# Optimization experiments

Hardware: AMD Instinct MI355X
Metric: run time of the kernel (lower is better)

The kernel has to match this reference:

```python
import jax, jax.numpy as jnp
import numpy as np

NUM_HEADS = 16
HEAD_DIM = 64
HIDDEN = NUM_HEADS * HEAD_DIM  # 1024
B, T = 32, 512


def setup_inputs() -> dict:
    key = jax.random.key(0)
    ks = jax.random.split(key, 10)
    s = 1.0 / np.sqrt(HIDDEN)
    inp = {
        "x": jax.random.normal(ks[0], (B, HIDDEN, T), dtype=jnp.float32),
        "mask": jax.random.randint(ks[1], (B, T), 0, 2, dtype=jnp.int32),
        "Wq": jax.random.uniform(ks[2], (HIDDEN, HIDDEN), jnp.float32, -s, s),
        "bq": jax.random.uniform(ks[3], (HIDDEN,), jnp.float32, -s, s),
        "Wk": jax.random.uniform(ks[4], (HIDDEN, HIDDEN), jnp.float32, -s, s),
        "bk": jax.random.uniform(ks[5], (HIDDEN,), jnp.float32, -s, s),
        "Wv": jax.random.uniform(ks[6], (HIDDEN, HIDDEN), jnp.float32, -s, s),
        "bv": jax.random.uniform(ks[7], (HIDDEN,), jnp.float32, -s, s),
        "Wo": jax.random.uniform(ks[8], (HIDDEN, HIDDEN), jnp.float32, -s, s),
        "bo": jax.random.uniform(ks[9], (HIDDEN,), jnp.float32, -s, s),
    }
    return inp


def reference(x, mask, Wq, bq, Wk, bk, Wv, bv, Wo, bo):
    # x: [B, hidden, T] -> tokens along last axis
    b, h, t = x.shape
    xt = jnp.swapaxes(x, 1, 2)  # [B, T, hidden]

    def heads(w, bias):
        y = xt @ w.T + bias                       # [B, T, hidden]
        return y.reshape(b, t, NUM_HEADS, HEAD_DIM).transpose(0, 2, 1, 3)  # [B, nh, T, hd]

    q = heads(Wq, bq)
    k = heads(Wk, bk)
    v = heads(Wv, bv)

    scores = jnp.einsum("bhqd,bhkd->bhqk", q, k) / jnp.sqrt(jnp.float32(HEAD_DIM))
    # masked_fill(mask==0, -inf) then clamp to [-50, 50]: masked entries become -50
    scores = jnp.where(mask[:, None, None, :] == 0, -jnp.inf, scores)
    scores = jnp.clip(scores, -50.0, 50.0)
    attn = jax.nn.softmax(scores, axis=-1)        # [B, nh, T, T]
    out = jnp.einsum("bhqk,bhkd->bhqd", attn, v)  # [B, nh, T, hd]
    out = out.transpose(0, 2, 1, 3).reshape(b, t, h)
    out = out @ Wo.T + bo                         # [B, T, hidden]
    return out.max(axis=1)                        # [B, hidden]
```

## Files before the change

kernel.cpp:

```cpp
#include <hip/hip_runtime.h>


typedef _Float16 half8 __attribute__((ext_vector_type(8)));
typedef _Float16 half4 __attribute__((ext_vector_type(4)));
typedef float floatx4 __attribute__((ext_vector_type(4)));
typedef unsigned uintx2 __attribute__((ext_vector_type(2)));

#define HID 1024
#define TT 512
#define NB 32
#define QSCALE 0.1803368801111244f
#define SB2 72.13475204444817f

__device__ __forceinline__ void gload16(const void* g, void* l) {
    __builtin_amdgcn_global_load_lds(
        (const __attribute__((address_space(1))) unsigned int*)g,
        (__attribute__((address_space(3))) unsigned int*)l, 16, 0, 0);
}

__device__ __forceinline__ unsigned fkey(float f) {
    unsigned u = __float_as_uint(f);
    return (u & 0x80000000u) ? ~u : (u | 0x80000000u);
}
__device__ __forceinline__ float funkey(unsigned k) {
    unsigned u = (k & 0x80000000u) ? (k ^ 0x80000000u) : ~k;
    return __uint_as_float(u);
}

__global__ __launch_bounds__(256) void prep_kernel(
    const float* __restrict__ Wq, const float* __restrict__ Wk,
    const float* __restrict__ Wv, const float* __restrict__ Wo,
    _Float16* __restrict__ Wcat,
    const float* __restrict__ x, _Float16* __restrict__ xT,
    unsigned* __restrict__ omax,
    const float* __restrict__ bq, float* __restrict__ bqs)
{
    __shared__ float tile[64][65];
    const int bid = blockIdx.x;
    if (bid < 4096) {
        int i4 = bid * 256 + threadIdx.x;
        int sec = i4 >> 18;
        int off4 = i4 & ((1 << 18) - 1);
        const float* src = (sec == 0) ? Wq : (sec == 1) ? Wk
                          : (sec == 2) ? Wv : Wo;
        float4 v = ((const float4*)src)[off4];
        if (sec == 0) {
            v.x *= QSCALE; v.y *= QSCALE; v.z *= QSCALE; v.w *= QSCALE;
        }
        half4 h = {(_Float16)v.x, (_Float16)v.y, (_Float16)v.z, (_Float16)v.w};
        *(half4*)(Wcat + (size_t)i4 * 4) = h;
    } else if (bid < 8192) {
        int idx = bid - 4096;
        int b = idx >> 7, h0 = ((idx >> 3) & 15) * 64, t0 = (idx & 7) * 64;
        int tx = threadIdx.x & 15, ty = threadIdx.x >> 4;
        const float* xb = x + ((size_t)b * HID + h0) * TT + t0;
        for (int p = 0; p < 4; p++) {
            int r = ty + 16 * p;
            float4 v = *(const float4*)(xb + (size_t)r * TT + tx * 4);
            tile[r][tx * 4 + 0] = v.x;
            tile[r][tx * 4 + 1] = v.y;
            tile[r][tx * 4 + 2] = v.z;
            tile[r][tx * 4 + 3] = v.w;
        }
        __syncthreads();
        int hc = (threadIdx.x & 7) * 8, tb = threadIdx.x >> 3;
        for (int rd = 0; rd < 2; rd++) {
            int tt = tb + 32 * rd;
            half8 pk;
            for (int k = 0; k < 8; k++)
                pk[k] = (_Float16)tile[hc + k][tt];
            *(half8*)(xT + ((size_t)b * TT + t0 + tt) * HID + h0 + hc) = pk;
        }
    } else if (bid < 8320) {
        omax[(bid - 8192) * 256 + threadIdx.x] = 0u;
    } else {
        int i = (bid - 8320) * 256 + threadIdx.x;
        bqs[i] = bq[i] * QSCALE;
    }
}


#define PH_PRE do { \
    __builtin_amdgcn_s_barrier(); \
    asm volatile("s_waitcnt lgkmcnt(0)" ::: "memory"); \
    __builtin_amdgcn_sched_barrier(0); \
    __builtin_amdgcn_s_setprio(1); \
} while (0)

#define PH_POST(N) do { \
    __builtin_amdgcn_s_setprio(0); \
    asm volatile("s_waitcnt vmcnt(" #N ")" ::: "memory"); \
    __builtin_amdgcn_s_barrier(); \
} while (0)

#define LDA(P, MH) do { \
    const _Float16* ab_ = lds + (P) * 16384 + (MH) * 8192 + aoff; \
    af[0][0] = *(const half8*)(ab_ + pb0); \
    af[0][1] = *(const half8*)(ab_ + pb1); \
    af[1][0] = *(const half8*)(ab_ + 1024 + pb0); \
    af[1][1] = *(const half8*)(ab_ + 1024 + pb1); \
    af[2][0] = *(const half8*)(ab_ + 2048 + pb0); \
    af[2][1] = *(const half8*)(ab_ + 2048 + pb1); \
    af[3][0] = *(const half8*)(ab_ + 3072 + pb0); \
    af[3][1] = *(const half8*)(ab_ + 3072 + pb1); \
} while (0)

#define LDB(P, NH) do { \
    const _Float16* bb_ = lds + 32768 + (P) * 16384 + (NH) * 8192 + boff; \
    bf[NH][0][0] = *(const half8*)(bb_ + pb0); \
    bf[NH][0][1] = *(const half8*)(bb_ + pb1); \
    bf[NH][1][0] = *(const half8*)(bb_ + 1024 + pb0); \
    bf[NH][1][1] = *(const half8*)(bb_ + 1024 + pb1); \
} while (0)

#define STAGE_A(P, MH, K0) do { \
    _Float16* d_ = lds + (P) * 16384 + (MH) * 8192 + wst; \
    gload16(ag + (MH) * 64 * 1024 + (K0), d_); \
    gload16(ag + (128 + (MH) * 64) * 1024 + (K0), d_ + 4096); \
} while (0)

#define STAGE_B(P, NH, K0) do { \
    _Float16* d_ = lds + 32768 + (P) * 16384 + (NH) * 8192 + wst; \
    gload16(bg + (NH) * 32 * 1024 + (K0), d_); \
    gload16(bg + (128 + (NH) * 32) * 1024 + (K0), d_ + 4096); \
} while (0)

#define MFMAQ(MH, NH) do { \
    _Pragma("unroll") \
    for (int j_ = 0; j_ < 4; ++j_) { \
        _Pragma("unroll") \
        for (int n_ = 0; n_ < 2; ++n_) { \
            floatx4 c_ = acc[(MH) * 4 + j_][(NH) * 2 + n_]; \
            c_ = __builtin_amdgcn_mfma_f32_16x16x32_f16( \
                af[j_][0], bf[NH][n_][0], c_, 0, 0, 0); \
            c_ = __builtin_amdgcn_mfma_f32_16x16x32_f16( \
                af[j_][1], bf[NH][n_][1], c_, 0, 0, 0); \
            acc[(MH) * 4 + j_][(NH) * 2 + n_] = c_; \
        } \
    } \
} while (0)

__device__ __forceinline__ void mainloop256(
    const _Float16* __restrict__ Ag,
    const _Float16* __restrict__ Bg,
    _Float16* lds, floatx4 acc[8][4], int tid)
{
    const int lane = tid & 63;
    const int w = tid >> 6, wr = w >> 2, wc = w & 3;
    const int l15 = lane & 15, quad = lane >> 4;
    const int pa = quad ^ (l15 & 7);
    const int pb0 = pa * 8, pb1 = (pa ^ 4) * 8;
    const int aoff = (wr * 64 + l15) * 64;
    const int boff = (wc * 32 + l15) * 64;
    const int wst = w * 512;
    const int r = tid >> 3;
    const int sg = (tid & 7) ^ (r & 7);
    const int nbase = ((r >> 5) << 6) + (r & 31);
    const _Float16* ag = Ag + (size_t)r * 1024 + sg * 8;
    const _Float16* bg = Bg + (size_t)nbase * 1024 + sg * 8;

    half8 af[4][2], bf[2][2][2];

    STAGE_A(0, 0, 0); STAGE_B(0, 0, 0); STAGE_B(0, 1, 0); STAGE_A(0, 1, 0);
    STAGE_A(1, 0, 64); STAGE_B(1, 0, 64); STAGE_B(1, 1, 64);
    asm volatile("s_waitcnt vmcnt(10)" ::: "memory");
    __builtin_amdgcn_s_barrier();

    for (int i = 0; i < 7; ++i) {
        const int kb = i * 128 + 64;
        const int kn0 = kb + 64, kn1 = kb + 128;
        LDA(0, 0); LDB(0, 0); STAGE_A(1, 1, kb);
        PH_PRE; MFMAQ(0, 0); PH_POST(10);
        LDB(0, 1);            STAGE_A(0, 0, kn0);
        PH_PRE; MFMAQ(0, 1); PH_POST(10);
        LDA(0, 1);            STAGE_B(0, 0, kn0);
        PH_PRE; MFMAQ(1, 1); PH_POST(10);
                              STAGE_B(0, 1, kn0);
        PH_PRE; MFMAQ(1, 0); PH_POST(10);
        LDA(1, 0); LDB(1, 0); STAGE_A(0, 1, kn0);
        PH_PRE; MFMAQ(0, 0); PH_POST(10);
        LDB(1, 1);            STAGE_A(1, 0, kn1);
        PH_PRE; MFMAQ(0, 1); PH_POST(10);
        LDA(1, 1);            STAGE_B(1, 0, kn1);
        PH_PRE; MFMAQ(1, 1); PH_POST(10);
                              STAGE_B(1, 1, kn1);
        PH_PRE; MFMAQ(1, 0); PH_POST(10);
    }
    LDA(0, 0); LDB(0, 0); STAGE_A(1, 1, 960);
    PH_PRE; MFMAQ(0, 0); PH_POST(10);
    LDB(0, 1);
    PH_PRE; MFMAQ(0, 1); PH_POST(8);
    LDA(0, 1);
    PH_PRE; MFMAQ(1, 1); PH_POST(6);
    PH_PRE; MFMAQ(1, 0); PH_POST(4);
    LDA(1, 0); LDB(1, 0);
    PH_PRE; MFMAQ(0, 0); PH_POST(2);
    LDB(1, 1);
    PH_PRE; MFMAQ(0, 1); PH_POST(0);
    LDA(1, 1);
    PH_PRE; MFMAQ(1, 1); MFMAQ(1, 0);
    __builtin_amdgcn_s_setprio(0);
}

__global__ __launch_bounds__(512, 2) void gemm1_kernel(
    const _Float16* __restrict__ Wcat,
    const float* __restrict__ bqs, const float* __restrict__ bk,
    const float* __restrict__ bv,
    const _Float16* __restrict__ xT,
    _Float16* __restrict__ QT, _Float16* __restrict__ KT,
    _Float16* __restrict__ Vb)
{
    __shared__ __align__(16) _Float16 smem[65536];
    const int tid = threadIdx.x;
    const int id = blockIdx.x;
    const int xcd = id & 7, slot = id >> 3;
    const int grp = xcd + 8 * (slot / 12);
    const int m0 = (slot % 12) * 256;
    const int n0 = (grp & 1) * 256;
    const int bb = grp >> 1;
    const int lane = tid & 63;
    const int w = tid >> 6, wr = w >> 2, wc = w & 3;
    const int l15 = lane & 15, quad = lane >> 4;

    floatx4 acc[8][4] = {};
    mainloop256(Wcat + (size_t)m0 * 1024,
                xT + ((size_t)bb * TT + n0) * HID, smem, acc, tid);
    __syncthreads();

    const int sec = m0 >> 10;
    const int mo = m0 & 1023;

    if (sec < 2) {
        const float* bias = (sec == 0) ? bqs : bk;
        _Float16* dst = (sec == 0) ? QT : KT;
        _Float16* tr = smem;
        for (int h = 0; h < 2; ++h) {
            if (wr == h) {
                for (int mi = 0; mi < 8; ++mi) {
                    float bs[4];
                    for (int rr = 0; rr < 4; ++rr)
                        bs[rr] = bias[mo + h * 128 + mi * 16 + quad * 4 + rr];
                    for (int ni = 0; ni < 4; ++ni) {
                        half4 pk;
                        for (int rr = 0; rr < 4; ++rr)
                            pk[rr] = (_Float16)(acc[mi][ni][rr] + bs[rr]);
                        *(half4*)(tr + (wc * 64 + ni * 16 + l15) * 136 +
                                  mi * 16 + quad * 4) = pk;
                    }
                }
            }
            __syncthreads();
            const int row = tid >> 4, off = (tid & 15) * 8;
            for (int s = 0; s < 8; ++s) {
                uint4 v = *(uint4*)(tr + (row + 32 * s) * 136 + off);
                *(uint4*)(dst + ((size_t)bb * TT + n0 + row + 32 * s) * HID +
                          mo + h * 128 + off) = v;
            }
            __syncthreads();
        }
    } else {
        for (int mi = 0; mi < 8; ++mi) {
            float bs[4];
            for (int rr = 0; rr < 4; ++rr)
                bs[rr] = bv[mo + wr * 128 + mi * 16 + quad * 4 + rr];
            for (int ni = 0; ni < 4; ++ni) {
                int t = n0 + wc * 64 + ni * 16 + l15;
                for (int rr = 0; rr < 4; ++rr) {
                    int o = mo + wr * 128 + mi * 16 + quad * 4 + rr;
                    Vb[((size_t)bb * HID + o) * TT + t] =
                        (_Float16)(acc[mi][ni][rr] + bs[rr]);
                }
            }
        }
    }
}

__global__ __launch_bounds__(256) void attn_kernel(
    const _Float16* __restrict__ QT, const _Float16* __restrict__ KT,
    const _Float16* __restrict__ Vb, const int* __restrict__ mask,
    _Float16* __restrict__ OcT)
{
    __shared__ __align__(16) _Float16 kvbuf[4 * 4096];
    __shared__ __align__(16) _Float16 ps[2 * 4096];
    __shared__ __align__(16) float msf[2][64];

    const int id = blockIdx.x;
    const int xcd = id & 7, slot = id >> 3;
    const int grp = xcd + 8 * (slot >> 2);
    const int q0 = (slot & 3) * 128;
    const int hd = grp & 15, b = grp >> 4;
    const int tid = threadIdx.x;
    const int lane = tid & 63, wid = tid >> 6;
    const int l15 = lane & 15, quad = lane >> 4;

    const _Float16* QTb = QT + ((size_t)b * TT + q0) * HID + hd * 64;
    const _Float16* KTb = KT + (size_t)b * TT * HID + hd * 64;
    const _Float16* Vbb = Vb + ((size_t)b * HID + hd * 64) * TT;
    const int* mb = mask + b * TT;

    const int srow = lane >> 3;
    const int sg = (lane & 7) ^ srow;
    const int pa = quad ^ (l15 & 7);
    const int pz = l15 & 7;

    for (int qt = 0; qt < 2; qt++)
        for (int p = 0; p < 2; p++) {
            int r = p * 32 + wid * 8 + srow;
            gload16(QTb + (size_t)(qt * 64 + r) * HID + sg * 8,
                    kvbuf + qt * 4096 + (p * 32 + wid * 8) * 64);
        }
    __syncthreads();
    half8 bq[2][2];
    for (int qt = 0; qt < 2; qt++) {
        bq[qt][0] = *(half8*)(kvbuf + qt * 4096 + (wid * 16 + l15) * 64 + pa * 8);
        bq[qt][1] = *(half8*)(kvbuf + qt * 4096 + (wid * 16 + l15) * 64 + (pa ^ 4) * 8);
    }
    __syncthreads();

    auto stage = [&](int jcn, int bufn) {
        int t0n = jcn * 64;
        _Float16* kd = kvbuf + bufn * 4096;
        _Float16* vd = kvbuf + (2 + bufn) * 4096;
        for (int p = 0; p < 2; p++) {
            int r = p * 32 + wid * 8 + srow;
            gload16(KTb + (size_t)(t0n + r) * HID + sg * 8,
                    kd + (p * 32 + wid * 8) * 64);
            gload16(Vbb + (size_t)r * TT + t0n + sg * 8,
                    vd + (p * 32 + wid * 8) * 64);
        }
        if (tid < 64) msf[bufn][tid] = mb[t0n + tid] ? SB2 : -SB2;
    };

    stage(0, 0);

    floatx4 oacc[2][4] = {};
    float rs[2] = {0.f, 0.f};
    const float lo = -SB2;

    for (int jc = 0; jc < 8; jc++) {
        const int cur = jc & 1;
        __syncthreads();
        if (jc < 7) stage(jc + 1, 1 - cur);

        const _Float16* ks = kvbuf + cur * 4096;
        const _Float16* vs = kvbuf + (2 + cur) * 4096;

        for (int jt = 0; jt < 4; jt++) {
            half8 ka0 = *(half8*)(ks + (jt * 16 + l15) * 64 + pa * 8);
            half8 ka1 = *(half8*)(ks + (jt * 16 + l15) * 64 + (pa ^ 4) * 8);
            floatx4 hi = *(floatx4*)(&msf[cur][jt * 16 + quad * 4]);
            for (int qt = 0; qt < 2; qt++) {
                floatx4 sc = {0.f, 0.f, 0.f, 0.f};
                sc = __builtin_amdgcn_mfma_f32_16x16x32_f16(ka0, bq[qt][0], sc, 0, 0, 0);
                sc = __builtin_amdgcn_mfma_f32_16x16x32_f16(ka1, bq[qt][1], sc, 0, 0, 0);
                float e0 = __builtin_amdgcn_exp2f(fminf(fmaxf(sc[0], lo), hi[0]));
                float e1 = __builtin_amdgcn_exp2f(fminf(fmaxf(sc[1], lo), hi[1]));
                float e2 = __builtin_amdgcn_exp2f(fminf(fmaxf(sc[2], lo), hi[2]));
                float e3 = __builtin_amdgcn_exp2f(fminf(fmaxf(sc[3], lo), hi[3]));
                rs[qt] += (e0 + e1) + (e2 + e3);
                unsigned uA = __builtin_bit_cast(
                    unsigned, __builtin_amdgcn_cvt_pkrtz(e0, e1));
                unsigned uB = __builtin_bit_cast(
                    unsigned, __builtin_amdgcn_cvt_pkrtz(e2, e3));
                uintx2 uv = {uA, uB};
                half4 pk = __builtin_bit_cast(half4, uv);
                int g = jt * 2 + (quad >> 1);
                *(half4*)(ps + qt * 4096 + (wid * 16 + l15) * 64 + (g ^ pz) * 8 +
                          (quad & 1) * 4) = pk;
            }
        }
        for (int kc = 0; kc < 2; kc++) {
            int g = kc * 4 + quad;
            half8 bv8[4];
            for (int d4 = 0; d4 < 4; d4++)
                bv8[d4] = *(half8*)(vs + (d4 * 16 + l15) * 64 + (g ^ pz) * 8);
            for (int qt = 0; qt < 2; qt++) {
                half8 ap = *(half8*)(ps + qt * 4096 + (wid * 16 + l15) * 64 +
                                     (g ^ pz) * 8);
                for (int d4 = 0; d4 < 4; d4++)
                    oacc[qt][d4] = __builtin_amdgcn_mfma_f32_16x16x32_f16(
                        ap, bv8[d4], oacc[qt][d4], 0, 0, 0);
            }
        }
    }

    for (int qt = 0; qt < 2; qt++) {
        float s = rs[qt];
        s += __shfl_xor(s, 16, 64);
        s += __shfl_xor(s, 32, 64);
        s = 1.0f / s;
        float inv[4];
        for (int r = 0; r < 4; r++) inv[r] = __shfl(s, quad * 4 + r, 64);
        for (int d4 = 0; d4 < 4; d4++)
            for (int r = 0; r < 4; r++) {
                int t = q0 + qt * 64 + wid * 16 + quad * 4 + r;
                int c = hd * 64 + d4 * 16 + l15;
                OcT[((size_t)b * TT + t) * HID + c] =
                    (_Float16)(oacc[qt][d4][r] * inv[r]);
            }
    }
}

__global__ __launch_bounds__(512, 2) void gemm2_kernel(
    const _Float16* __restrict__ Wo16, const _Float16* __restrict__ OcT,
    unsigned* __restrict__ omax)
{
    __shared__ __align__(16) _Float16 smem[65536];
    const int tid = threadIdx.x;
    const int id = blockIdx.x;
    const int xcd = id & 7, slot = id >> 3;
    const int grp = xcd + 8 * (slot >> 2);
    const int m0 = (slot & 3) * 256;
    const int n0 = (grp & 1) * 256;
    const int bb = grp >> 1;
    const int lane = tid & 63;
    const int w = tid >> 6, wr = w >> 2;
    const int l15 = lane & 15, quad = lane >> 4;

    floatx4 acc[8][4] = {};
    mainloop256(Wo16 + (size_t)m0 * 1024,
                OcT + ((size_t)bb * TT + n0) * HID, smem, acc, tid);

    for (int mi = 0; mi < 8; ++mi)
        for (int rr = 0; rr < 4; ++rr) {
            float v = acc[mi][0][rr];
            v = fmaxf(v, acc[mi][1][rr]);
            v = fmaxf(v, acc[mi][2][rr]);
            v = fmaxf(v, acc[mi][3][rr]);
            for (int d = 1; d < 16; d <<= 1)
                v = fmaxf(v, __shfl_xor(v, d, 64));
            if (l15 == 0) {
                int o = m0 + wr * 128 + mi * 16 + quad * 4 + rr;
                atomicMax(&omax[bb * HID + o], fkey(v));
            }
        }
}

__global__ __launch_bounds__(256) void final_kernel(
    const unsigned* __restrict__ omax, const float* __restrict__ bo,
    float* __restrict__ out)
{
    int i = blockIdx.x * 256 + threadIdx.x;
    out[i] = funkey(omax[i]) + bo[i & 1023];
}

extern "C" void kernel_launch(void* const* d_in, const int* in_sizes, int n_in,
                              void* d_out, int out_size, void* d_ws, size_t ws_size,
                              hipStream_t stream)
{
    const float* x  = (const float*)d_in[0];
    const int* mask = (const int*)d_in[1];
    const float* Wq = (const float*)d_in[2];
    const float* bq = (const float*)d_in[3];
    const float* Wk = (const float*)d_in[4];
    const float* bk = (const float*)d_in[5];
    const float* Wv = (const float*)d_in[6];
    const float* bv = (const float*)d_in[7];
    const float* Wo = (const float*)d_in[8];
    const float* bo = (const float*)d_in[9];
    float* out = (float*)d_out;

    char* ws = (char*)d_ws;
    _Float16* Wcat = (_Float16*)(ws);
    _Float16* xT   = (_Float16*)(ws + (8ull  << 20));
    _Float16* QT   = (_Float16*)(ws + (40ull << 20));
    _Float16* KT   = (_Float16*)(ws + (72ull << 20));
    _Float16* Vb   = (_Float16*)(ws + (104ull << 20));
    _Float16* OcT  = (_Float16*)(ws + (136ull << 20));
    unsigned* omax = (unsigned*)(ws + (168ull << 20));
    float*    bqs  = (float*)(ws + (168ull << 20) + (128ull << 10));

    prep_kernel<<<8324, 256, 0, stream>>>(Wq, Wk, Wv, Wo, Wcat, x, xT, omax,
                                          bq, bqs);
    gemm1_kernel<<<768, 512, 0, stream>>>(Wcat, bqs, bk, bv, xT, QT, KT, Vb);
    attn_kernel<<<2048, 256, 0, stream>>>(QT, KT, Vb, mask, OcT);
    gemm2_kernel<<<256, 512, 0, stream>>>(Wcat + (3ull << 20), OcT, omax);
    final_kernel<<<128, 256, 0, stream>>>(omax, bo, out);
}
```

Measured before the change: 325.0 us.

## Make gemm1 persistent over three M tiles with streaming pipeline across tiles

Each gemm1 block now handles three consecutive 256-row M tiles (grid drops from 768 to 256 blocks) and runs one continuous 48-step K pipeline. The global-to-LDS prefetch of the next tile starts while the current tile finishes, and epilogues run between tiles. The Q/K epilogue writes directly to global with half4 stores instead of transposing through LDS, which removes barriers but gives less coalesced stores. The goals are to hide pipeline ramp-up and drain per tile and to drop per-block launch overhead, at the cost of fewer blocks (256 on a 256-CU part) and possible load imbalance.

New measurement: 315.8 us. 2.8% less time.

```diff
diff --git a/kernel.cpp b/kernel.cpp
--- a/kernel.cpp
+++ b/kernel.cpp
@@ -79,7 +79,6 @@
     }
 }
 
-
 #define PH_PRE do { \
     __builtin_amdgcn_s_barrier(); \
     asm volatile("s_waitcnt lgkmcnt(0)" ::: "memory"); \
@@ -111,18 +110,6 @@
     bf[NH][0][1] = *(const half8*)(bb_ + pb1); \
     bf[NH][1][0] = *(const half8*)(bb_ + 1024 + pb0); \
     bf[NH][1][1] = *(const half8*)(bb_ + 1024 + pb1); \
-} while (0)
-
-#define STAGE_A(P, MH, K0) do { \
-    _Float16* d_ = lds + (P) * 16384 + (MH) * 8192 + wst; \
-    gload16(ag + (MH) * 64 * 1024 + (K0), d_); \
-    gload16(ag + (128 + (MH) * 64) * 1024 + (K0), d_ + 4096); \
-} while (0)
-
-#define STAGE_B(P, NH, K0) do { \
-    _Float16* d_ = lds + 32768 + (P) * 16384 + (NH) * 8192 + wst; \
-    gload16(bg + (NH) * 32 * 1024 + (K0), d_); \
-    gload16(bg + (128 + (NH) * 32) * 1024 + (K0), d_ + 4096); \
 } while (0)
 
 #define MFMAQ(MH, NH) do { \
@@ -138,6 +125,18 @@
             acc[(MH) * 4 + j_][(NH) * 2 + n_] = c_; \
         } \
     } \
+} while (0)
+
+#define STAGE_A(P, MH, K0) do { \
+    _Float16* d_ = lds + (P) * 16384 + (MH) * 8192 + wst; \
+    gload16(ag + (MH) * 65536 + (K0), d_); \
+    gload16(ag + 131072 + (MH) * 65536 + (K0), d_ + 4096); \
+} while (0)
+
+#define STAGE_B(P, NH, K0) do { \
+    _Float16* d_ = lds + 32768 + (P) * 16384 + (NH) * 8192 + wst; \
+    gload16(bg + (NH) * 32768 + (K0), d_); \
+    gload16(bg + 131072 + (NH) * 32768 + (K0), d_ + 4096); \
 } while (0)
 
 __device__ __forceinline__ void mainloop256(
@@ -202,6 +201,41 @@
     __builtin_amdgcn_s_setprio(0);
 }
 
+#define AOF(J) (((J) >> 4) * 262144 + ((J) & 15) * 64)
+#define BOF(J) (((J) & 15) * 64)
+
+#define SA1(P, MH, J) do { \
+    _Float16* d_ = lds + (P) * 16384 + (MH) * 8192 + wst; \
+    gload16(ag + (MH) * 65536 + AOF(J), d_); \
+    gload16(ag + 131072 + (MH) * 65536 + AOF(J), d_ + 4096); \
+} while (0)
+
+#define SB1(P, NH, J) do { \
+    _Float16* d_ = lds + 32768 + (P) * 16384 + (NH) * 8192 + wst; \
+    gload16(bg + (NH) * 32768 + BOF(J), d_); \
+    gload16(bg + 131072 + (NH) * 32768 + BOF(J), d_ + 4096); \
+} while (0)
+
+#define PAIR(I) do { \
+    const int j1 = 2 * (I) + 1, j2 = 2 * (I) + 2, j3 = 2 * (I) + 3; \
+    LDA(0, 0); LDB(0, 0); SA1(1, 1, j1); \
+    PH_PRE; MFMAQ(0, 0); PH_POST(10); \
+    LDB(0, 1);            SA1(0, 0, j2); \
+    PH_PRE; MFMAQ(0, 1); PH_POST(10); \
+    LDA(0, 1);            SB1(0, 0, j2); \
+    PH_PRE; MFMAQ(1, 1); PH_POST(10); \
+                          SB1(0, 1, j2); \
+    PH_PRE; MFMAQ(1, 0); PH_POST(10); \
+    LDA(1, 0); LDB(1, 0); SA1(0, 1, j2); \
+    PH_PRE; MFMAQ(0, 0); PH_POST(10); \
+    LDB(1, 1);            SA1(1, 0, j3); \
+    PH_PRE; MFMAQ(0, 1); PH_POST(10); \
+    LDA(1, 1);            SB1(1, 0, j3); \
+    PH_PRE; MFMAQ(1, 1); PH_POST(10); \
+                          SB1(1, 1, j3); \
+    PH_PRE; MFMAQ(1, 0); PH_POST(10); \
+} while (0)
+
 __global__ __launch_bounds__(512, 2) void gemm1_kernel(
     const _Float16* __restrict__ Wcat,
     const float* __restrict__ bqs, const float* __restrict__ bk,
@@ -211,68 +245,95 @@
     _Float16* __restrict__ Vb)
 {
     __shared__ __align__(16) _Float16 smem[65536];
+    _Float16* lds = smem;
     const int tid = threadIdx.x;
     const int id = blockIdx.x;
     const int xcd = id & 7, slot = id >> 3;
-    const int grp = xcd + 8 * (slot / 12);
-    const int m0 = (slot % 12) * 256;
+    const int grp = xcd + 8 * (slot >> 2);
+    const int mseg = slot & 3;
     const int n0 = (grp & 1) * 256;
     const int bb = grp >> 1;
     const int lane = tid & 63;
     const int w = tid >> 6, wr = w >> 2, wc = w & 3;
     const int l15 = lane & 15, quad = lane >> 4;
+    const int pa = quad ^ (l15 & 7);
+    const int pb0 = pa * 8, pb1 = (pa ^ 4) * 8;
+    const int aoff = (wr * 64 + l15) * 64;
+    const int boff = (wc * 32 + l15) * 64;
+    const int wst = w * 512;
+    const int r = tid >> 3;
+    const int sg = (tid & 7) ^ (r & 7);
+    const int nbase = ((r >> 5) << 6) + (r & 31);
+    const _Float16* ag = Wcat + (size_t)(mseg * 768 + r) * 1024 + sg * 8;
+    const _Float16* bg = xT + ((size_t)bb * TT + n0 + nbase) * 1024 + sg * 8;
 
     floatx4 acc[8][4] = {};
-    mainloop256(Wcat + (size_t)m0 * 1024,
-                xT + ((size_t)bb * TT + n0) * HID, smem, acc, tid);
-    __syncthreads();
-
-    const int sec = m0 >> 10;
-    const int mo = m0 & 1023;
-
-    if (sec < 2) {
-        const float* bias = (sec == 0) ? bqs : bk;
-        _Float16* dst = (sec == 0) ? QT : KT;
-        _Float16* tr = smem;
-        for (int h = 0; h < 2; ++h) {
-            if (wr == h) {
-                for (int mi = 0; mi < 8; ++mi) {
-                    float bs[4];
+    half8 af[4][2], bf[2][2][2];
+
+    auto epi = [&](int v) {
+        const int mt = mseg * 3 + v;
+        const int sec = mt >> 2;
+        const int mo = (mt & 3) * 256 + wr * 128;
+        if (sec < 2) {
+            const float* bias = (sec == 0) ? bqs : bk;
+            _Float16* dst = (sec == 0) ? QT : KT;
+            _Float16* drow = dst + ((size_t)bb * TT + n0 + wc * 64 + l15) * HID
+                             + mo + quad * 4;
+            for (int mi = 0; mi < 8; ++mi) {
+                float bs[4];
+                for (int rr = 0; rr < 4; ++rr)
+                    bs[rr] = bias[mo + mi * 16 + quad * 4 + rr];
+                for (int ni = 0; ni < 4; ++ni) {
+                    half4 pk;
                     for (int rr = 0; rr < 4; ++rr)
-                        bs[rr] = bias[mo + h * 128 + mi * 16 + quad * 4 + rr];
-                    for (int ni = 0; ni < 4; ++ni) {
-                        half4 pk;
-                        for (int rr = 0; rr < 4; ++rr)
-                            pk[rr] = (_Float16)(acc[mi][ni][rr] + bs[rr]);
-                        *(half4*)(tr + (wc * 64 + ni * 16 + l15) * 136 +
-                                  mi * 16 + quad * 4) = pk;
-                    }
+                        pk[rr] = (_Float16)(acc[mi][ni][rr] + bs[rr]);
+                    *(half4*)(drow + (size_t)(ni * 16) * HID + mi * 16) = pk;
+                    acc[mi][ni] = (floatx4){0.f, 0.f, 0.f, 0.f};
                 }
             }
-            __syncthreads();
-            const int row = tid >> 4, off = (tid & 15) * 8;
-            for (int s = 0; s < 8; ++s) {
-                uint4 v = *(uint4*)(tr + (row + 32 * s) * 136 + off);
-                *(uint4*)(dst + ((size_t)bb * TT + n0 + row + 32 * s) * HID +
-                          mo + h * 128 + off) = v;
-            }
-            __syncthreads();
-        }
-    } else {
-        for (int mi = 0; mi < 8; ++mi) {
-            float bs[4];
-            for (int rr = 0; rr < 4; ++rr)
-                bs[rr] = bv[mo + wr * 128 + mi * 16 + quad * 4 + rr];
-            for (int ni = 0; ni < 4; ++ni) {
-                int t = n0 + wc * 64 + ni * 16 + l15;
-                for (int rr = 0; rr < 4; ++rr) {
-                    int o = mo + wr * 128 + mi * 16 + quad * 4 + rr;
-                    Vb[((size_t)bb * HID + o) * TT + t] =
-                        (_Float16)(acc[mi][ni][rr] + bs[rr]);
+        } else {
+            for (int mi = 0; mi < 8; ++mi) {
+                float bs[4];
+                for (int rr = 0; rr < 4; ++rr)
+                    bs[rr] = bv[mo + mi * 16 + quad * 4 + rr];
+                for (int ni = 0; ni < 4; ++ni) {
+                    int t = n0 + wc * 64 + ni * 16 + l15;
+                    for (int rr = 0; rr < 4; ++rr) {
+                        int o = mo + mi * 16 + quad * 4 + rr;
+                        Vb[((size_t)bb * HID + o) * TT + t] =
+                            (_Float16)(acc[mi][ni][rr] + bs[rr]);
+                    }
+                    acc[mi][ni] = (floatx4){0.f, 0.f, 0.f, 0.f};
                 }
             }
         }
-    }
+    };
+
+    SA1(0, 0, 0); SB1(0, 0, 0); SB1(0, 1, 0); SA1(0, 1, 0);
+    SA1(1, 0, 1); SB1(1, 0, 1); SB1(1, 1, 1);
+    asm volatile("s_waitcnt vmcnt(10)" ::: "memory");
+    __builtin_amdgcn_s_barrier();
+
+    for (int ii = 0; ii < 8; ++ii) PAIR(ii);
+    epi(0);
+    for (int ii = 8; ii < 16; ++ii) PAIR(ii);
+    epi(1);
+    for (int ii = 16; ii < 23; ++ii) PAIR(ii);
+    LDA(0, 0); LDB(0, 0); SA1(1, 1, 47);
+    PH_PRE; MFMAQ(0, 0); PH_POST(10);
+    LDB(0, 1);
+    PH_PRE; MFMAQ(0, 1); PH_POST(8);
+    LDA(0, 1);
+    PH_PRE; MFMAQ(1, 1); PH_POST(6);
+    PH_PRE; MFMAQ(1, 0); PH_POST(4);
+    LDA(1, 0); LDB(1, 0);
+    PH_PRE; MFMAQ(0, 0); PH_POST(2);
+    LDB(1, 1);
+    PH_PRE; MFMAQ(0, 1); PH_POST(0);
+    LDA(1, 1);
+    PH_PRE; MFMAQ(1, 1); MFMAQ(1, 0);
+    __builtin_amdgcn_s_setprio(0);
+    epi(2);
 }
 
 __global__ __launch_bounds__(256) void attn_kernel(
@@ -406,6 +467,7 @@
     unsigned* __restrict__ omax)
 {
     __shared__ __align__(16) _Float16 smem[65536];
+    _Float16* lds = smem;
     const int tid = threadIdx.x;
     const int id = blockIdx.x;
     const int xcd = id & 7, slot = id >> 3;
@@ -419,7 +481,7 @@
 
     floatx4 acc[8][4] = {};
     mainloop256(Wo16 + (size_t)m0 * 1024,
-                OcT + ((size_t)bb * TT + n0) * HID, smem, acc, tid);
+                OcT + ((size_t)bb * TT + n0) * HID, lds, acc, tid);
 
     for (int mi = 0; mi < 8; ++mi)
         for (int rr = 0; rr < 4; ++rr) {
@@ -472,7 +534,7 @@
 
     prep_kernel<<<8324, 256, 0, stream>>>(Wq, Wk, Wv, Wo, Wcat, x, xT, omax,
                                           bq, bqs);
-    gemm1_kernel<<<768, 512, 0, stream>>>(Wcat, bqs, bk, bv, xT, QT, KT, Vb);
+    gemm1_kernel<<<256, 512, 0, stream>>>(Wcat, bqs, bk, bv, xT, QT, KT, Vb);
     attn_kernel<<<2048, 256, 0, stream>>>(QT, KT, Vb, mask, OcT);
     gemm2_kernel<<<256, 512, 0, stream>>>(Wcat + (3ull << 20), OcT, omax);
     final_kernel<<<128, 256, 0, stream>>>(omax, bo, out);
```

## Enlarge attention blocks to 512 threads covering 256 queries each

Applied to the files above, without the earlier changes.

The attention kernel now runs 1024 blocks of 512 threads, each handling 256 query rows of one (batch, head) instead of 128 rows with 256 threads. Each staged K/V tile in LDS is therefore shared by twice as many queries, which halves global K/V traffic and per-block staging work. The probability buffer doubles in size and launch bounds are raised to (512, 4). That tighter bound caps registers per thread and could cause spilling or lower MFMA efficiency. The STAGE macros are only reordered and their constants pre-folded.

Result: no change. 321.6 us (-1.0%).

```diff
diff --git a/kernel.cpp b/kernel.cpp
--- a/kernel.cpp
+++ b/kernel.cpp
@@ -79,7 +79,6 @@
     }
 }
 
-
 #define PH_PRE do { \
     __builtin_amdgcn_s_barrier(); \
     asm volatile("s_waitcnt lgkmcnt(0)" ::: "memory"); \
@@ -111,18 +110,6 @@
     bf[NH][0][1] = *(const half8*)(bb_ + pb1); \
     bf[NH][1][0] = *(const half8*)(bb_ + 1024 + pb0); \
     bf[NH][1][1] = *(const half8*)(bb_ + 1024 + pb1); \
-} while (0)
-
-#define STAGE_A(P, MH, K0) do { \
-    _Float16* d_ = lds + (P) * 16384 + (MH) * 8192 + wst; \
-    gload16(ag + (MH) * 64 * 1024 + (K0), d_); \
-    gload16(ag + (128 + (MH) * 64) * 1024 + (K0), d_ + 4096); \
-} while (0)
-
-#define STAGE_B(P, NH, K0) do { \
-    _Float16* d_ = lds + 32768 + (P) * 16384 + (NH) * 8192 + wst; \
-    gload16(bg + (NH) * 32 * 1024 + (K0), d_); \
-    gload16(bg + (128 + (NH) * 32) * 1024 + (K0), d_ + 4096); \
 } while (0)
 
 #define MFMAQ(MH, NH) do { \
@@ -138,6 +125,18 @@
             acc[(MH) * 4 + j_][(NH) * 2 + n_] = c_; \
         } \
     } \
+} while (0)
+
+#define STAGE_A(P, MH, K0) do { \
+    _Float16* d_ = lds + (P) * 16384 + (MH) * 8192 + wst; \
+    gload16(ag + (MH) * 65536 + (K0), d_); \
+    gload16(ag + 131072 + (MH) * 65536 + (K0), d_ + 4096); \
+} while (0)
+
+#define STAGE_B(P, NH, K0) do { \
+    _Float16* d_ = lds + 32768 + (P) * 16384 + (NH) * 8192 + wst; \
+    gload16(bg + (NH) * 32768 + (K0), d_); \
+    gload16(bg + 131072 + (NH) * 32768 + (K0), d_ + 4096); \
 } while (0)
 
 __device__ __forceinline__ void mainloop256(
@@ -275,19 +274,19 @@
     }
 }
 
-__global__ __launch_bounds__(256) void attn_kernel(
+__global__ __launch_bounds__(512, 4) void attn_kernel(
     const _Float16* __restrict__ QT, const _Float16* __restrict__ KT,
     const _Float16* __restrict__ Vb, const int* __restrict__ mask,
     _Float16* __restrict__ OcT)
 {
     __shared__ __align__(16) _Float16 kvbuf[4 * 4096];
-    __shared__ __align__(16) _Float16 ps[2 * 4096];
+    __shared__ __align__(16) _Float16 ps[2 * 8192];
     __shared__ __align__(16) float msf[2][64];
 
     const int id = blockIdx.x;
     const int xcd = id & 7, slot = id >> 3;
-    const int grp = xcd + 8 * (slot >> 2);
-    const int q0 = (slot & 3) * 128;
+    const int grp = xcd + 8 * (slot >> 1);
+    const int q0 = (slot & 1) * 256;
     const int hd = grp & 15, b = grp >> 4;
     const int tid = threadIdx.x;
     const int lane = tid & 63, wid = tid >> 6;
@@ -303,17 +302,17 @@
     const int pa = quad ^ (l15 & 7);
     const int pz = l15 & 7;
 
-    for (int qt = 0; qt < 2; qt++)
-        for (int p = 0; p < 2; p++) {
-            int r = p * 32 + wid * 8 + srow;
-            gload16(QTb + (size_t)(qt * 64 + r) * HID + sg * 8,
-                    kvbuf + qt * 4096 + (p * 32 + wid * 8) * 64);
-        }
+    for (int p = 0; p < 4; p++) {
+        int r = p * 64 + wid * 8 + srow;
+        gload16(QTb + (size_t)r * HID + sg * 8,
+                kvbuf + (p * 64 + wid * 8) * 64);
+    }
     __syncthreads();
     half8 bq[2][2];
     for (int qt = 0; qt < 2; qt++) {
-        bq[qt][0] = *(half8*)(kvbuf + qt * 4096 + (wid * 16 + l15) * 64 + pa * 8);
-        bq[qt][1] = *(half8*)(kvbuf + qt * 4096 + (wid * 16 + l15) * 64 + (pa ^ 4) * 8);
+        int qr = qt * 128 + wid * 16 + l15;
+        bq[qt][0] = *(half8*)(kvbuf + qr * 64 + pa * 8);
+        bq[qt][1] = *(half8*)(kvbuf + qr * 64 + (pa ^ 4) * 8);
     }
     __syncthreads();
 
@@ -321,13 +320,9 @@
         int t0n = jcn * 64;
         _Float16* kd = kvbuf + bufn * 4096;
         _Float16* vd = kvbuf + (2 + bufn) * 4096;
-        for (int p = 0; p < 2; p++) {
-            int r = p * 32 + wid * 8 + srow;
-            gload16(KTb + (size_t)(t0n + r) * HID + sg * 8,
-                    kd + (p * 32 + wid * 8) * 64);
-            gload16(Vbb + (size_t)r * TT + t0n + sg * 8,
-                    vd + (p * 32 + wid * 8) * 64);
-        }
+        int r = wid * 8 + srow;
+        gload16(KTb + (size_t)(t0n + r) * HID + sg * 8, kd + (wid * 8) * 64);
+        gload16(Vbb + (size_t)r * TT + t0n + sg * 8, vd + (wid * 8) * 64);
         if (tid < 64) msf[bufn][tid] = mb[t0n + tid] ? SB2 : -SB2;
     };
 
@@ -365,7 +360,7 @@
                 uintx2 uv = {uA, uB};
                 half4 pk = __builtin_bit_cast(half4, uv);
                 int g = jt * 2 + (quad >> 1);
-                *(half4*)(ps + qt * 4096 + (wid * 16 + l15) * 64 + (g ^ pz) * 8 +
+                *(half4*)(ps + qt * 8192 + (wid * 16 + l15) * 64 + (g ^ pz) * 8 +
                           (quad & 1) * 4) = pk;
             }
         }
@@ -375,7 +370,7 @@
             for (int d4 = 0; d4 < 4; d4++)
                 bv8[d4] = *(half8*)(vs + (d4 * 16 + l15) * 64 + (g ^ pz) * 8);
             for (int qt = 0; qt < 2; qt++) {
-                half8 ap = *(half8*)(ps + qt * 4096 + (wid * 16 + l15) * 64 +
+                half8 ap = *(half8*)(ps + qt * 8192 + (wid * 16 + l15) * 64 +
                                      (g ^ pz) * 8);
                 for (int d4 = 0; d4 < 4; d4++)
                     oacc[qt][d4] = __builtin_amdgcn_mfma_f32_16x16x32_f16(
@@ -393,7 +388,7 @@
         for (int r = 0; r < 4; r++) inv[r] = __shfl(s, quad * 4 + r, 64);
         for (int d4 = 0; d4 < 4; d4++)
             for (int r = 0; r < 4; r++) {
-                int t = q0 + qt * 64 + wid * 16 + quad * 4 + r;
+                int t = q0 + qt * 128 + wid * 16 + quad * 4 + r;
                 int c = hd * 64 + d4 * 16 + l15;
                 OcT[((size_t)b * TT + t) * HID + c] =
                     (_Float16)(oacc[qt][d4][r] * inv[r]);
@@ -406,6 +401,7 @@
     unsigned* __restrict__ omax)
 {
     __shared__ __align__(16) _Float16 smem[65536];
+    _Float16* lds = smem;
     const int tid = threadIdx.x;
     const int id = blockIdx.x;
     const int xcd = id & 7, slot = id >> 3;
@@ -419,7 +415,7 @@
 
     floatx4 acc[8][4] = {};
     mainloop256(Wo16 + (size_t)m0 * 1024,
-                OcT + ((size_t)bb * TT + n0) * HID, smem, acc, tid);
+                OcT + ((size_t)bb * TT + n0) * HID, lds, acc, tid);
 
     for (int mi = 0; mi < 8; ++mi)
         for (int rr = 0; rr < 4; ++rr) {
@@ -473,7 +469,7 @@
     prep_kernel<<<8324, 256, 0, stream>>>(Wq, Wk, Wv, Wo, Wcat, x, xT, omax,
                                           bq, bqs);
     gemm1_kernel<<<768, 512, 0, stream>>>(Wcat, bqs, bk, bv, xT, QT, KT, Vb);
-    attn_kernel<<<2048, 256, 0, stream>>>(QT, KT, Vb, mask, OcT);
+    attn_kernel<<<1024, 512, 0, stream>>>(QT, KT, Vb, mask, OcT);
     gemm2_kernel<<<256, 512, 0, stream>>>(Wcat + (3ull << 20), OcT, omax);
     final_kernel<<<128, 256, 0, stream>>>(omax, bo, out);
 }
```
